# Optimization experiments

Hardware: AMD Instinct MI355X
Metric: run time of the kernel (lower is better)

## Reference

```python
import jax, jax.numpy as jnp
import numpy as np

B, T, C, H = 4, 2048, 2048, 16
HD = C // H


def apply_rope(x, cos, sin):
    d = x.shape[-1]
    neg_half = jnp.concatenate([-x[..., d // 2:], x[..., :d // 2]], axis=-1)
    return x * cos + neg_half * sin


def setup_inputs() -> dict:
    key = jax.random.key(0)
    ks = jax.random.split(key, 12)
    s = 1.0 / np.sqrt(C)
    return {
        "x": jax.random.normal(ks[0], (B, T, C), jnp.float32),
        "cos": jax.random.uniform(ks[1], (T, C), jnp.float32),
        "sin": jax.random.uniform(ks[2], (T, C), jnp.float32),
        "Wq": jax.random.normal(ks[3], (C, C), jnp.float32) * s,
        "bq": jnp.zeros((C,), jnp.float32),
        "Wk": jax.random.normal(ks[4], (C, C), jnp.float32) * s,
        "bk": jnp.zeros((C,), jnp.float32),
        "Wv": jax.random.normal(ks[5], (C, C), jnp.float32) * s,
        "bv": jnp.zeros((C,), jnp.float32),
        "Wo": jax.random.normal(ks[6], (C, C), jnp.float32) * s,
        "bo": jnp.zeros((C,), jnp.float32),
    }


def reference(x, cos, sin, Wq, bq, Wk, bk, Wv, bv, Wo, bo):
    # projections (torch Linear: x @ W.T + b)
    q = x @ Wq.T + bq
    k = x @ Wk.T + bk
    v = x @ Wv.T + bv
    # kv cache stores PRE-RoPE k and v (as in the original)
    k_new, v_new = k, v
    # RoPE on the full embedding dim, before head split
    q = apply_rope(q, cos[:T], sin[:T])
    k = apply_rope(k, cos[:T], sin[:T])
    # split heads -> [B, H, T, HD]
    qh = q.reshape(B, T, H, HD).transpose(0, 2, 1, 3)
    kh = k.reshape(B, T, H, HD).transpose(0, 2, 1, 3)
    vh = v.reshape(B, T, H, HD).transpose(0, 2, 1, 3)
    scores = jnp.einsum("bhqd,bhkd->bhqk", qh, kh) / jnp.sqrt(jnp.float32(HD))
    causal = jnp.tril(jnp.ones((T, T), bool))
    scores = jnp.where(causal, scores, jnp.float32(-jnp.inf))
    attn = jax.nn.softmax(scores, axis=-1)
    out = jnp.einsum("bhqk,bhkd->bhqd", attn, vh)
    out = out.transpose(0, 2, 1, 3).reshape(B, T, C)
    out = out @ Wo.T + bo
    return (out, k_new, v_new)
```

## Files before the change

kernel.cpp:

```cpp
#include <hip/hip_runtime.h>

typedef unsigned short u16;
typedef unsigned int u32;

typedef __attribute__((ext_vector_type(8))) short bf16x8;
typedef __attribute__((ext_vector_type(4))) float f32x4;
typedef __attribute__((ext_vector_type(16))) float f32x16;
typedef __attribute__((ext_vector_type(4))) u32 u32x4;

__device__ __forceinline__ u16 f2bf(float f) {
  u32 u = __builtin_bit_cast(u32, f);
  u32 r = (u + 0x7fffu + ((u >> 16) & 1u)) >> 16;
  return (u16)r;
}
__device__ __forceinline__ float bf2f(u16 h) {
  return __builtin_bit_cast(float, (u32)h << 16);
}
__device__ __forceinline__ u32 cvtpk(float lo, float hi) {
  u32 d;
  asm("v_cvt_pk_bf16_f32 %0, %1, %2" : "=v"(d) : "v"(lo), "v"(hi));
  return d;
}
__device__ __forceinline__ void plswap(u32& a, u32& b) {
  asm("v_permlane32_swap_b32 %0, %1" : "+v"(a), "+v"(b));
}

#define GLD16(g, l)                                       \
  __builtin_amdgcn_global_load_lds(                       \
      (__attribute__((address_space(1))) void*)(g),       \
      (__attribute__((address_space(3))) void*)(l), 16, 0, 0)

#define WAITV8() asm volatile("s_waitcnt vmcnt(8)" ::: "memory")
#define WAITV0() asm volatile("s_waitcnt vmcnt(0)" ::: "memory")
#define BARF()                               \
  {                                          \
    asm volatile("" ::: "memory");           \
    __builtin_amdgcn_s_barrier();            \
    asm volatile("" ::: "memory");           \
  }

__global__ __launch_bounds__(256) void cvt_bf16(const float* __restrict__ src,
                                                u16* __restrict__ dst, int n4) {
  int i = blockIdx.x * 256 + threadIdx.x;
  if (i >= n4) return;
  float4 v = ((const float4*)src)[i];
  ushort4 o;
  o.x = f2bf(v.x); o.y = f2bf(v.y); o.z = f2bf(v.z); o.w = f2bf(v.w);
  ((ushort4*)dst)[i] = o;
}

__global__ __launch_bounds__(256) void cvt_w4(const float* __restrict__ s0,
                                              const float* __restrict__ s1,
                                              const float* __restrict__ s2,
                                              const float* __restrict__ s3,
                                              u16* __restrict__ d0,
                                              u16* __restrict__ d1,
                                              u16* __restrict__ d2,
                                              u16* __restrict__ d3) {
  int j = blockIdx.x >> 12;
  int i = (blockIdx.x & 4095) * 256 + threadIdx.x;
  const float* src = (j == 0) ? s0 : (j == 1) ? s1 : (j == 2) ? s2 : s3;
  u16* dst = (j == 0) ? d0 : (j == 1) ? d1 : (j == 2) ? d2 : d3;
  float4 v = ((const float4*)src)[i];
  ushort4 o;
  o.x = f2bf(v.x); o.y = f2bf(v.y); o.z = f2bf(v.z); o.w = f2bf(v.w);
  ((ushort4*)dst)[i] = o;
}

__global__ __launch_bounds__(256) void rope2(u16* __restrict__ qb,
                                             u16* __restrict__ kb,
                                             const float* __restrict__ cosT,
                                             const float* __restrict__ sinT,
                                             float scaleQ) {
  int i = blockIdx.x * 256 + threadIdx.x;
  int c4 = (i & 255) << 2;
  size_t bt = (size_t)(i >> 8);
  int t = (int)(bt & 2047);
  float4 c1 = *(const float4*)&cosT[(size_t)t * 2048 + c4];
  float4 s1 = *(const float4*)&sinT[(size_t)t * 2048 + c4];
  float4 c2 = *(const float4*)&cosT[(size_t)t * 2048 + c4 + 1024];
  float4 s2 = *(const float4*)&sinT[(size_t)t * 2048 + c4 + 1024];
#pragma unroll
  for (int which = 0; which < 2; which++) {
    u16* buf = which ? kb : qb;
    float scale = which ? 1.0f : scaleQ;
    u16* p1 = buf + bt * 2048 + c4;
    u16* p2 = p1 + 1024;
    ushort4 x1 = *(const ushort4*)p1;
    ushort4 x2 = *(const ushort4*)p2;
    float a0 = bf2f(x1.x), a1 = bf2f(x1.y), a2 = bf2f(x1.z), a3 = bf2f(x1.w);
    float b0 = bf2f(x2.x), b1 = bf2f(x2.y), b2 = bf2f(x2.z), b3 = bf2f(x2.w);
    ushort4 o1, o2;
    o1.x = f2bf((a0 * c1.x - b0 * s1.x) * scale);
    o1.y = f2bf((a1 * c1.y - b1 * s1.y) * scale);
    o1.z = f2bf((a2 * c1.z - b2 * s1.z) * scale);
    o1.w = f2bf((a3 * c1.w - b3 * s1.w) * scale);
    o2.x = f2bf((b0 * c2.x + a0 * s2.x) * scale);
    o2.y = f2bf((b1 * c2.y + a1 * s2.y) * scale);
    o2.z = f2bf((b2 * c2.z + a2 * s2.z) * scale);
    o2.w = f2bf((b3 * c2.w + a3 * s2.w) * scale);
    *(ushort4*)p1 = o1;
    *(ushort4*)p2 = o2;
  }
}

__global__ __launch_bounds__(512, 2) void gemm_bt(const u16* __restrict__ A,
                                                  const u16* __restrict__ Wm,
                                                  const float* __restrict__ bias,
                                                  float* __restrict__ outF,
                                                  u16* __restrict__ outB,
                                                  u16* __restrict__ outT) {
  __shared__ __attribute__((aligned(16))) char L[131072];
  const int tid = threadIdx.x;
  const int lane = tid & 63;
  const int w = tid >> 6;
  const int wr = w >> 2;
  const int wcn = w & 3;
  const int lin = blockIdx.y * 8 + blockIdx.x;
  const int swz = ((lin & 7) << 5) | (lin >> 3);
  const int m0 = (swz >> 3) * 256, n0 = (swz & 7) * 256;
  const int r15 = lane & 15, rg = lane >> 4;
  const int sw = (r15 & 7) << 4;

  const int trow = tid >> 3;
  const int tlog = ((tid & 7) << 4) ^ ((trow & 7) << 4);
  const u16* pA = A + (size_t)(m0 + trow) * 2048 + (tlog >> 1);
  const u16* pB = Wm + (size_t)(n0 + trow) * 2048 + (tlog >> 1);
  char* dA = L + tid * 16;
  char* dB = L + 65536 + tid * 16;

#define STAGE(dst, src, koff)                                   \
  {                                                             \
    _Pragma("unroll")                                           \
    for (int c = 0; c < 4; c++)                                 \
      GLD16((src) + (size_t)c * 131072 + (koff), (dst) + c * 8192); \
  }

  const char* aBase = L + wr * 16384;
  const char* bBase = L + 65536 + (wcn >> 1) * 16384 + (wcn & 1) * 8192;

  f32x4 acc[8][4] = {};
  bf16x8 ar[4][2], br[2][2][2];

  auto LD_A = [&](int mq, int soff) {
#pragma unroll
    for (int mf = 0; mf < 4; mf++)
#pragma unroll
      for (int ks = 0; ks < 2; ks++) {
        int row = mq * 64 + mf * 16 + r15;
        ar[mf][ks] = *(const bf16x8*)(aBase + soff + row * 128 +
                                      ((ks * 64 + rg * 16) ^ sw));
      }
  };
  auto LD_B = [&](int nq, int soff) {
#pragma unroll
    for (int nf = 0; nf < 2; nf++)
#pragma unroll
      for (int ks = 0; ks < 2; ks++) {
        int row = nq * 32 + nf * 16 + r15;
        br[nq][nf][ks] = *(const bf16x8*)(bBase + soff + row * 128 +
                                          ((ks * 64 + rg * 16) ^ sw));
      }
  };
  auto QUAD = [&](int mq, int nq) {
#pragma unroll
    for (int mf = 0; mf < 4; mf++)
#pragma unroll
      for (int nf = 0; nf < 2; nf++)
#pragma unroll
        for (int ks = 0; ks < 2; ks++)
          acc[mq * 4 + mf][nq * 2 + nf] = __builtin_amdgcn_mfma_f32_16x16x32_bf16(
              ar[mf][ks], br[nq][nf][ks], acc[mq * 4 + mf][nq * 2 + nf], 0, 0, 0);
  };
  auto COMPUTE = [&](int soff) {
    LD_A(0, soff);
    LD_B(0, soff);
    LD_B(1, soff);
    __builtin_amdgcn_s_setprio(1);
    QUAD(0, 0);
    QUAD(0, 1);
    __builtin_amdgcn_s_setprio(0);
    LD_A(1, soff);
    __builtin_amdgcn_s_setprio(1);
    QUAD(1, 1);
    QUAD(1, 0);
    __builtin_amdgcn_s_setprio(0);
  };

  STAGE(dA, pA, 0);
  STAGE(dB, pB, 0);
  asm volatile("" ::: "memory");
  STAGE(dA + 32768, pA, 64);
  STAGE(dB + 32768, pB, 64);
  WAITV8();
  BARF();

  for (int it = 0; it < 16; it++) {
    COMPUTE(0);
    BARF();
    if (it < 15) {
      STAGE(dA, pA, (2 * it + 2) * 64);
      STAGE(dB, pB, (2 * it + 2) * 64);
      WAITV8();
    } else {
      WAITV0();
    }
    BARF();
    COMPUTE(32768);
    if (it < 15) {
      BARF();
      STAGE(dA + 32768, pA, (2 * it + 3) * 64);
      STAGE(dB + 32768, pB, (2 * it + 3) * 64);
      WAITV8();
      BARF();
    }
  }

#pragma unroll
  for (int am = 0; am < 8; am++)
#pragma unroll
    for (int bn = 0; bn < 4; bn++) {
      int n = n0 + wcn * 64 + bn * 16 + r15;
      float bs = bias[n];
#pragma unroll
      for (int i = 0; i < 4; i++) {
        int m = m0 + wr * 128 + am * 16 + rg * 4 + i;
        float v = acc[am][bn][i] + bs;
        if (outF) outF[(size_t)m * 2048 + n] = v;
        if (outB) outB[(size_t)m * 2048 + n] = f2bf(v);
        if (outT) {
          int b_ = m >> 11, t_ = m & 2047, h_ = n >> 7, d_ = n & 127;
          outT[(((size_t)(b_ * 16 + h_) * 128 + d_) << 11) + t_] = f2bf(v);
        }
      }
    }
#undef STAGE
}

__global__ __launch_bounds__(256, 2) void attn_fwd(const u16* __restrict__ Qb,
                                                   const u16* __restrict__ Kb,
                                                   const u16* __restrict__ Vt,
                                                   u16* __restrict__ AO) {
  __shared__ __attribute__((aligned(16))) u16 Ks[2][64 * 128];
  __shared__ __attribute__((aligned(16))) u16 Vs[2][64 * 128];
  const int tid = threadIdx.x;
  const int lane = tid & 63;
  const int w = tid >> 6;
  const int c31 = lane & 31, hi = lane >> 5;
  const int bh = blockIdx.y;
  const int b = bh >> 4, h = bh & 15;
  const int p = blockIdx.x;

  const u16* ksrc[4];
  const u16* vsrc[4];
  int xoff[4];
#pragma unroll
  for (int c = 0; c < 4; c++) {
    int X = c * 4096 + tid * 16;
    int row = X >> 8, phys = X & 255;
    int lg = phys ^ ((row & 15) << 4);
    xoff[c] = X;
    ksrc[c] = Kb + (size_t)(b * 2048 + row) * 2048 + h * 128 + (lg >> 1);
    int vd = row + ((lg >> 7) << 6);
    int kvb = lg & 127;
    vsrc[c] = Vt + ((size_t)(b * 16 + h) * 128 + vd) * 2048 + (kvb >> 1);
  }

  for (int phase = 0; phase < 2; phase++) {
    const int q0 = (phase == 0 ? (15 - p) : p) * 128;
    const int qw0 = q0 + w * 32;
    const int q = qw0 + c31;

    bf16x8 qreg[8];
    {
      const u16* qp = Qb + ((size_t)(b * 2048 + q)) * 2048 + h * 128 + hi * 8;
#pragma unroll
      for (int ks = 0; ks < 8; ks++) qreg[ks] = *(const bf16x8*)(qp + ks * 16);
    }

    f32x16 accO[4] = {};
    float m_run = -__builtin_inff(), l_run = 0.f;
    const int ntiles = (q0 >> 6) + 2;

    __syncthreads();
#pragma unroll
    for (int c = 0; c < 4; c++) {
      GLD16(ksrc[c], (char*)Ks + xoff[c]);
      GLD16(vsrc[c], (char*)Vs + xoff[c]);
    }

    for (int it = 0; it < ntiles; it++) {
      const int kv0 = it << 6;
      const int buf = it & 1;
      __syncthreads();
      if (it + 1 < ntiles) {
        const int nb = buf ^ 1;
        const int kvn = (it + 1) << 6;
#pragma unroll
        for (int c = 0; c < 4; c++) {
          GLD16(ksrc[c] + (size_t)kvn * 2048, (char*)Ks + nb * 16384 + xoff[c]);
          GLD16(vsrc[c] + kvn, (char*)Vs + nb * 16384 + xoff[c]);
        }
      }
      if (kv0 > qw0 + 31) continue;

      f32x16 sT[2] = {};
      {
        const char* kb = (const char*)Ks + buf * 16384;
#pragma unroll
        for (int kvt = 0; kvt < 2; kvt++) {
          int krow = kvt * 32 + c31;
          const char* kr = kb + krow * 256;
          int swz = (krow & 15) << 4;
#pragma unroll
          for (int ks = 0; ks < 8; ks++) {
            bf16x8 kf = *(const bf16x8*)(kr + ((ks * 32 + hi * 16) ^ swz));
            sT[kvt] = __builtin_amdgcn_mfma_f32_32x32x16_bf16(kf, qreg[ks], sT[kvt], 0, 0, 0);
          }
        }
      }

      if (kv0 + 63 > qw0) {
#pragma unroll
        for (int kvt = 0; kvt < 2; kvt++)
#pragma unroll
          for (int r = 0; r < 16; r++) {
            int kv = kv0 + kvt * 32 + (r & 3) + 8 * (r >> 2) + 4 * hi;
            if (kv > q) sT[kvt][r] = -__builtin_inff();
          }
      }

      float tm[16];
#pragma unroll
      for (int r = 0; r < 16; r++) tm[r] = fmaxf(sT[0][r], sT[1][r]);
#pragma unroll
      for (int st = 8; st > 0; st >>= 1)
#pragma unroll
        for (int r = 0; r < st; r++) tm[r] = fmaxf(tm[r], tm[r + st]);
      float pmax = tm[0];
      pmax = fmaxf(pmax, __shfl_xor(pmax, 32));

      if (!__all(pmax - m_run <= 8.0f)) {
        float mnew = fmaxf(m_run, pmax);
        float alpha = exp2f(m_run - mnew);
        m_run = mnew;
        l_run *= alpha;
#pragma unroll
        for (int r = 0; r < 16; r++) {
          float ar = __shfl(alpha, (r & 3) + 8 * (r >> 2) + 4 * hi);
#pragma unroll
          for (int dt = 0; dt < 4; dt++) accO[dt][r] *= ar;
        }
      }

      float a0 = 0.f, a1 = 0.f, a2 = 0.f, a3 = 0.f;
#pragma unroll
      for (int kvt = 0; kvt < 2; kvt++)
#pragma unroll
        for (int r = 0; r < 16; r++) {
          float pv = exp2f(sT[kvt][r] - m_run);
          sT[kvt][r] = pv;
          if ((r & 3) == 0) a0 += pv; else if ((r & 3) == 1) a1 += pv;
          else if ((r & 3) == 2) a2 += pv; else a3 += pv;
        }
      float rs = (a0 + a1) + (a2 + a3);
      rs += __shfl_xor(rs, 32);
      l_run += rs;

      u32x4 pa[4];
#pragma unroll
      for (int kvt = 0; kvt < 2; kvt++)
#pragma unroll
        for (int hf = 0; hf < 2; hf++) {
          u32 wA0 = cvtpk(sT[kvt][hf * 8 + 0], sT[kvt][hf * 8 + 1]);
          u32 wA1 = cvtpk(sT[kvt][hf * 8 + 4], sT[kvt][hf * 8 + 5]);
          u32 wB0 = cvtpk(sT[kvt][hf * 8 + 2], sT[kvt][hf * 8 + 3]);
          u32 wB1 = cvtpk(sT[kvt][hf * 8 + 6], sT[kvt][hf * 8 + 7]);
          plswap(wA0, wA1);
          plswap(wB0, wB1);
          pa[kvt * 2 + hf] = (u32x4){wA0, wB0, wA1, wB1};
        }

      {
        const char* vb = (const char*)Vs + buf * 16384;
#pragma unroll
        for (int dt = 0; dt < 4; dt++) {
          int vrow = (dt & 1) * 32 + c31;
          const char* vr = vb + vrow * 256;
          int swz = (vrow & 15) << 4;
          int hsel = (dt >> 1) * 128;
#pragma unroll
          for (int ks = 0; ks < 4; ks++) {
            bf16x8 vf = *(const bf16x8*)(vr + ((hsel + ks * 32 + hi * 16) ^ swz));
            bf16x8 paf = __builtin_bit_cast(bf16x8, pa[ks]);
            accO[dt] = __builtin_amdgcn_mfma_f32_32x32x16_bf16(paf, vf, accO[dt], 0, 0, 0);
          }
        }
      }
    }

    float linv = 1.0f / l_run;
#pragma unroll
    for (int r = 0; r < 16; r++) {
      int crow = (r & 3) + 8 * (r >> 2) + 4 * hi;
      float lr = __shfl(linv, crow);
      int qq = qw0 + crow;
      u16* op = AO + (size_t)(b * 2048 + qq) * 2048 + h * 128 + c31;
#pragma unroll
      for (int dt = 0; dt < 4; dt++) op[dt * 32] = f2bf(accO[dt][r] * lr);
    }
  }
}

extern "C" void kernel_launch(void* const* d_in, const int* in_sizes, int n_in,
                              void* d_out, int out_size, void* d_ws, size_t ws_size,
                              hipStream_t stream) {
  const float* x    = (const float*)d_in[0];
  const float* cosT = (const float*)d_in[1];
  const float* sinT = (const float*)d_in[2];
  const float* Wq   = (const float*)d_in[3];
  const float* bq   = (const float*)d_in[4];
  const float* Wk   = (const float*)d_in[5];
  const float* bk   = (const float*)d_in[6];
  const float* Wv   = (const float*)d_in[7];
  const float* bv   = (const float*)d_in[8];
  const float* Wo   = (const float*)d_in[9];
  const float* bo   = (const float*)d_in[10];

  float* out   = (float*)d_out;
  float* k_new = out + (size_t)16777216;
  float* v_new = out + (size_t)33554432;

  char* ws = (char*)d_ws;
  u16* xb  = (u16*)(ws);
  u16* Wqb = (u16*)(ws + 33554432);
  u16* Wkb = (u16*)(ws + 41943040);
  u16* Wvb = (u16*)(ws + 50331648);
  u16* Wob = (u16*)(ws + 58720256);
  u16* Qb  = (u16*)(ws + 67108864);
  u16* Kb  = (u16*)(ws + 100663296);
  u16* Vt  = (u16*)(ws + 134217728);
  u16* AO  = xb;

  cvt_bf16<<<16384, 256, 0, stream>>>(x, xb, 4194304);
  cvt_w4<<<16384, 256, 0, stream>>>(Wq, Wk, Wv, Wo, Wqb, Wkb, Wvb, Wob);

  dim3 gg(8, 32);
  gemm_bt<<<gg, 512, 0, stream>>>(xb, Wqb, bq, nullptr, Qb, nullptr);
  gemm_bt<<<gg, 512, 0, stream>>>(xb, Wkb, bk, k_new, Kb, nullptr);
  gemm_bt<<<gg, 512, 0, stream>>>(xb, Wvb, bv, v_new, nullptr, Vt);

  const float sc2 = 1.44269504088896f * 0.08838834764831845f;
  rope2<<<8192, 256, 0, stream>>>(Qb, Kb, cosT, sinT, sc2);

  attn_fwd<<<dim3(8, 64), 256, 0, stream>>>(Qb, Kb, Vt, AO);

  gemm_bt<<<gg, 512, 0, stream>>>(AO, Wob, bo, out, nullptr, nullptr);
}
```

Before: 475.4 us.

## Fuse Q/K/V projections into one GEMM launch and enlarge attention blocks

The three separate Q, K and V projection GEMMs become one launch over a 24x32 tile grid. Each tile selects its bias and output format (bf16 Q, fp32+bf16 K, fp32+transposed bf16 V) by which weight segment it covers, which relies on Wq/Wk/Wv being contiguous in the workspace. The attention kernel moves to 512 threads with 256-query blocks sharing K/V tiles, halving per-thread loads and the block count. This removes launch gaps and tail effects and increases K/V reuse, but the larger attention blocks carry more idle causal work and lower occupancy.

```diff
diff --git a/kernel.cpp b/kernel.cpp
--- a/kernel.cpp
+++ b/kernel.cpp
@@ -104,30 +104,91 @@
   }
 }
 
-__global__ __launch_bounds__(512, 2) void gemm_bt(const u16* __restrict__ A,
-                                                  const u16* __restrict__ Wm,
-                                                  const float* __restrict__ bias,
-                                                  float* __restrict__ outF,
-                                                  u16* __restrict__ outB,
-                                                  u16* __restrict__ outT) {
-  __shared__ __attribute__((aligned(16))) char L[131072];
-  const int tid = threadIdx.x;
-  const int lane = tid & 63;
-  const int w = tid >> 6;
-  const int wr = w >> 2;
-  const int wcn = w & 3;
-  const int lin = blockIdx.y * 8 + blockIdx.x;
-  const int swz = ((lin & 7) << 5) | (lin >> 3);
-  const int m0 = (swz >> 3) * 256, n0 = (swz & 7) * 256;
-  const int r15 = lane & 15, rg = lane >> 4;
-  const int sw = (r15 & 7) << 4;
-
-  const int trow = tid >> 3;
-  const int tlog = ((tid & 7) << 4) ^ ((trow & 7) << 4);
-  const u16* pA = A + (size_t)(m0 + trow) * 2048 + (tlog >> 1);
-  const u16* pB = Wm + (size_t)(n0 + trow) * 2048 + (tlog >> 1);
-  char* dA = L + tid * 16;
-  char* dB = L + 65536 + tid * 16;
+#define GEMM_CORE(Aptr, Wptr)                                                  \
+  __shared__ __attribute__((aligned(16))) char L[131072];                      \
+  const int tid = threadIdx.x;                                                 \
+  const int lane = tid & 63;                                                   \
+  const int w = tid >> 6;                                                      \
+  const int wr = w >> 2;                                                       \
+  const int wcn = w & 3;                                                       \
+  const int r15 = lane & 15, rg = lane >> 4;                                   \
+  const int sw = (r15 & 7) << 4;                                               \
+  const int trow = tid >> 3;                                                   \
+  const int tlog = ((tid & 7) << 4) ^ ((trow & 7) << 4);                       \
+  const u16* pA = (Aptr) + (size_t)(m0 + trow) * 2048 + (tlog >> 1);           \
+  const u16* pB = (Wptr) + (size_t)(n0 + trow) * 2048 + (tlog >> 1);           \
+  char* dA = L + tid * 16;                                                     \
+  char* dB = L + 65536 + tid * 16;                                             \
+  const char* aBase = L + wr * 16384;                                          \
+  const char* bBase = L + 65536 + (wcn >> 1) * 16384 + (wcn & 1) * 8192;       \
+  f32x4 acc[8][4] = {};                                                        \
+  bf16x8 ar[4][2], br[2][2][2];                                                \
+  auto LD_A = [&](int mq, int soff) {                                          \
+    _Pragma("unroll") for (int mf = 0; mf < 4; mf++)                           \
+        _Pragma("unroll") for (int ks = 0; ks < 2; ks++) {                     \
+      int row = mq * 64 + mf * 16 + r15;                                       \
+      ar[mf][ks] = *(const bf16x8*)(aBase + soff + row * 128 +                 \
+                                    ((ks * 64 + rg * 16) ^ sw));               \
+    }                                                                          \
+  };                                                                           \
+  auto LD_B = [&](int nq, int soff) {                                          \
+    _Pragma("unroll") for (int nf = 0; nf < 2; nf++)                           \
+        _Pragma("unroll") for (int ks = 0; ks < 2; ks++) {                     \
+      int row = nq * 32 + nf * 16 + r15;                                       \
+      br[nq][nf][ks] = *(const bf16x8*)(bBase + soff + row * 128 +             \
+                                        ((ks * 64 + rg * 16) ^ sw));           \
+    }                                                                          \
+  };                                                                           \
+  auto QUAD = [&](int mq, int nq) {                                            \
+    _Pragma("unroll") for (int mf = 0; mf < 4; mf++)                           \
+        _Pragma("unroll") for (int nf = 0; nf < 2; nf++)                       \
+            _Pragma("unroll") for (int ks = 0; ks < 2; ks++)                   \
+        acc[mq * 4 + mf][nq * 2 + nf] =                                        \
+            __builtin_amdgcn_mfma_f32_16x16x32_bf16(                           \
+                ar[mf][ks], br[nq][nf][ks], acc[mq * 4 + mf][nq * 2 + nf],     \
+                0, 0, 0);                                                      \
+  };                                                                           \
+  auto COMPUTE = [&](int soff) {                                               \
+    LD_A(0, soff);                                                             \
+    LD_B(0, soff);                                                             \
+    LD_B(1, soff);                                                             \
+    __builtin_amdgcn_s_setprio(1);                                             \
+    QUAD(0, 0);                                                                \
+    QUAD(0, 1);                                                                \
+    __builtin_amdgcn_s_setprio(0);                                             \
+    LD_A(1, soff);                                                             \
+    __builtin_amdgcn_s_setprio(1);                                             \
+    QUAD(1, 1);                                                                \
+    QUAD(1, 0);                                                                \
+    __builtin_amdgcn_s_setprio(0);                                             \
+  };                                                                           \
+  STAGE(dA, pA, 0);                                                            \
+  STAGE(dB, pB, 0);                                                            \
+  asm volatile("" ::: "memory");                                               \
+  STAGE(dA + 32768, pA, 64);                                                   \
+  STAGE(dB + 32768, pB, 64);                                                   \
+  WAITV8();                                                                    \
+  BARF();                                                                      \
+  for (int it = 0; it < 16; it++) {                                            \
+    COMPUTE(0);                                                                \
+    BARF();                                                                    \
+    if (it < 15) {                                                             \
+      STAGE(dA, pA, (2 * it + 2) * 64);                                        \
+      STAGE(dB, pB, (2 * it + 2) * 64);                                        \
+      WAITV8();                                                                \
+    } else {                                                                   \
+      WAITV0();                                                                \
+    }                                                                          \
+    BARF();                                                                    \
+    COMPUTE(32768);                                                            \
+    if (it < 15) {                                                             \
+      BARF();                                                                  \
+      STAGE(dA + 32768, pA, (2 * it + 3) * 64);                                \
+      STAGE(dB + 32768, pB, (2 * it + 3) * 64);                                \
+      WAITV8();                                                                \
+      BARF();                                                                  \
+    }                                                                          \
+  }
 
 #define STAGE(dst, src, koff)                                   \
   {                                                             \
@@ -136,86 +197,55 @@
       GLD16((src) + (size_t)c * 131072 + (koff), (dst) + c * 8192); \
   }
 
-  const char* aBase = L + wr * 16384;
-  const char* bBase = L + 65536 + (wcn >> 1) * 16384 + (wcn & 1) * 8192;
-
-  f32x4 acc[8][4] = {};
-  bf16x8 ar[4][2], br[2][2][2];
-
-  auto LD_A = [&](int mq, int soff) {
-#pragma unroll
-    for (int mf = 0; mf < 4; mf++)
-#pragma unroll
-      for (int ks = 0; ks < 2; ks++) {
-        int row = mq * 64 + mf * 16 + r15;
-        ar[mf][ks] = *(const bf16x8*)(aBase + soff + row * 128 +
-                                      ((ks * 64 + rg * 16) ^ sw));
-      }
-  };
-  auto LD_B = [&](int nq, int soff) {
-#pragma unroll
-    for (int nf = 0; nf < 2; nf++)
-#pragma unroll
-      for (int ks = 0; ks < 2; ks++) {
-        int row = nq * 32 + nf * 16 + r15;
-        br[nq][nf][ks] = *(const bf16x8*)(bBase + soff + row * 128 +
-                                          ((ks * 64 + rg * 16) ^ sw));
-      }
-  };
-  auto QUAD = [&](int mq, int nq) {
-#pragma unroll
-    for (int mf = 0; mf < 4; mf++)
-#pragma unroll
-      for (int nf = 0; nf < 2; nf++)
-#pragma unroll
-        for (int ks = 0; ks < 2; ks++)
-          acc[mq * 4 + mf][nq * 2 + nf] = __builtin_amdgcn_mfma_f32_16x16x32_bf16(
-              ar[mf][ks], br[nq][nf][ks], acc[mq * 4 + mf][nq * 2 + nf], 0, 0, 0);
-  };
-  auto COMPUTE = [&](int soff) {
-    LD_A(0, soff);
-    LD_B(0, soff);
-    LD_B(1, soff);
-    __builtin_amdgcn_s_setprio(1);
-    QUAD(0, 0);
-    QUAD(0, 1);
-    __builtin_amdgcn_s_setprio(0);
-    LD_A(1, soff);
-    __builtin_amdgcn_s_setprio(1);
-    QUAD(1, 1);
-    QUAD(1, 0);
-    __builtin_amdgcn_s_setprio(0);
-  };
-
-  STAGE(dA, pA, 0);
-  STAGE(dB, pB, 0);
-  asm volatile("" ::: "memory");
-  STAGE(dA + 32768, pA, 64);
-  STAGE(dB + 32768, pB, 64);
-  WAITV8();
-  BARF();
-
-  for (int it = 0; it < 16; it++) {
-    COMPUTE(0);
-    BARF();
-    if (it < 15) {
-      STAGE(dA, pA, (2 * it + 2) * 64);
-      STAGE(dB, pB, (2 * it + 2) * 64);
-      WAITV8();
-    } else {
-      WAITV0();
-    }
-    BARF();
-    COMPUTE(32768);
-    if (it < 15) {
-      BARF();
-      STAGE(dA + 32768, pA, (2 * it + 3) * 64);
-      STAGE(dB + 32768, pB, (2 * it + 3) * 64);
-      WAITV8();
-      BARF();
-    }
-  }
-
+__global__ __launch_bounds__(512, 2) void gemm_qkv(const u16* __restrict__ A,
+                                                   const u16* __restrict__ Wqkv,
+                                                   const float* __restrict__ bq,
+                                                   const float* __restrict__ bk,
+                                                   const float* __restrict__ bv,
+                                                   u16* __restrict__ Qb,
+                                                   float* __restrict__ k_new,
+                                                   u16* __restrict__ Kb,
+                                                   float* __restrict__ v_new,
+                                                   u16* __restrict__ Vt) {
+  const int lin = blockIdx.y * 24 + blockIdx.x;
+  const int swz = (lin & 7) * 96 + (lin >> 3);
+  const int m0 = (swz / 24) * 256, n0 = (swz % 24) * 256;
+  GEMM_CORE(A, Wqkv)
+  const int seg = n0 >> 11;
+  const float* bias = (seg == 0) ? bq : (seg == 1) ? bk : bv;
+#pragma unroll
+  for (int am = 0; am < 8; am++)
+#pragma unroll
+    for (int bn = 0; bn < 4; bn++) {
+      int n = n0 + wcn * 64 + bn * 16 + r15;
+      int nl = n & 2047;
+      float bs = bias[nl];
+#pragma unroll
+      for (int i = 0; i < 4; i++) {
+        int m = m0 + wr * 128 + am * 16 + rg * 4 + i;
+        float v = acc[am][bn][i] + bs;
+        if (seg == 0) {
+          Qb[(size_t)m * 2048 + nl] = f2bf(v);
+        } else if (seg == 1) {
+          k_new[(size_t)m * 2048 + nl] = v;
+          Kb[(size_t)m * 2048 + nl] = f2bf(v);
+        } else {
+          v_new[(size_t)m * 2048 + nl] = v;
+          int b_ = m >> 11, t_ = m & 2047, h_ = nl >> 7, d_ = nl & 127;
+          Vt[(((size_t)(b_ * 16 + h_) * 128 + d_) << 11) + t_] = f2bf(v);
+        }
+      }
+    }
+}
+
+__global__ __launch_bounds__(512, 2) void gemm_bt(const u16* __restrict__ A,
+                                                  const u16* __restrict__ Wm,
+                                                  const float* __restrict__ bias,
+                                                  float* __restrict__ outF) {
+  const int lin = blockIdx.y * 8 + blockIdx.x;
+  const int swzb = ((lin & 7) << 5) | (lin >> 3);
+  const int m0 = (swzb >> 3) * 256, n0 = (swzb & 7) * 256;
+  GEMM_CORE(A, Wm)
 #pragma unroll
   for (int am = 0; am < 8; am++)
 #pragma unroll
@@ -225,19 +255,14 @@
 #pragma unroll
       for (int i = 0; i < 4; i++) {
         int m = m0 + wr * 128 + am * 16 + rg * 4 + i;
-        float v = acc[am][bn][i] + bs;
-        if (outF) outF[(size_t)m * 2048 + n] = v;
-        if (outB) outB[(size_t)m * 2048 + n] = f2bf(v);
-        if (outT) {
-          int b_ = m >> 11, t_ = m & 2047, h_ = n >> 7, d_ = n & 127;
-          outT[(((size_t)(b_ * 16 + h_) * 128 + d_) << 11) + t_] = f2bf(v);
-        }
-      }
-    }
+        outF[(size_t)m * 2048 + n] = acc[am][bn][i] + bs;
+      }
+    }
+}
 #undef STAGE
-}
-
-__global__ __launch_bounds__(256, 2) void attn_fwd(const u16* __restrict__ Qb,
+#undef GEMM_CORE
+
+__global__ __launch_bounds__(512, 2) void attn_fwd(const u16* __restrict__ Qb,
                                                    const u16* __restrict__ Kb,
                                                    const u16* __restrict__ Vt,
                                                    u16* __restrict__ AO) {
@@ -251,12 +276,12 @@
   const int b = bh >> 4, h = bh & 15;
   const int p = blockIdx.x;
 
-  const u16* ksrc[4];
-  const u16* vsrc[4];
-  int xoff[4];
-#pragma unroll
-  for (int c = 0; c < 4; c++) {
-    int X = c * 4096 + tid * 16;
+  const u16* ksrc[2];
+  const u16* vsrc[2];
+  int xoff[2];
+#pragma unroll
+  for (int c = 0; c < 2; c++) {
+    int X = c * 8192 + tid * 16;
     int row = X >> 8, phys = X & 255;
     int lg = phys ^ ((row & 15) << 4);
     xoff[c] = X;
@@ -267,7 +292,7 @@
   }
 
   for (int phase = 0; phase < 2; phase++) {
-    const int q0 = (phase == 0 ? (15 - p) : p) * 128;
+    const int q0 = (phase == 0 ? (7 - p) : p) * 256;
     const int qw0 = q0 + w * 32;
     const int q = qw0 + c31;
 
@@ -280,11 +305,11 @@
 
     f32x16 accO[4] = {};
     float m_run = -__builtin_inff(), l_run = 0.f;
-    const int ntiles = (q0 >> 6) + 2;
+    const int ntiles = (q0 >> 6) + 4;
 
     __syncthreads();
 #pragma unroll
-    for (int c = 0; c < 4; c++) {
+    for (int c = 0; c < 2; c++) {
       GLD16(ksrc[c], (char*)Ks + xoff[c]);
       GLD16(vsrc[c], (char*)Vs + xoff[c]);
     }
@@ -297,7 +322,7 @@
         const int nb = buf ^ 1;
         const int kvn = (it + 1) << 6;
 #pragma unroll
-        for (int c = 0; c < 4; c++) {
+        for (int c = 0; c < 2; c++) {
           GLD16(ksrc[c] + (size_t)kvn * 2048, (char*)Ks + nb * 16384 + xoff[c]);
           GLD16(vsrc[c] + kvn, (char*)Vs + nb * 16384 + xoff[c]);
         }
@@ -445,15 +470,13 @@
   cvt_bf16<<<16384, 256, 0, stream>>>(x, xb, 4194304);
   cvt_w4<<<16384, 256, 0, stream>>>(Wq, Wk, Wv, Wo, Wqb, Wkb, Wvb, Wob);
 
-  dim3 gg(8, 32);
-  gemm_bt<<<gg, 512, 0, stream>>>(xb, Wqb, bq, nullptr, Qb, nullptr);
-  gemm_bt<<<gg, 512, 0, stream>>>(xb, Wkb, bk, k_new, Kb, nullptr);
-  gemm_bt<<<gg, 512, 0, stream>>>(xb, Wvb, bv, v_new, nullptr, Vt);
+  gemm_qkv<<<dim3(24, 32), 512, 0, stream>>>(xb, Wqb, bq, bk, bv,
+                                             Qb, k_new, Kb, v_new, Vt);
 
   const float sc2 = 1.44269504088896f * 0.08838834764831845f;
   rope2<<<8192, 256, 0, stream>>>(Qb, Kb, cosT, sinT, sc2);
 
-  attn_fwd<<<dim3(8, 64), 256, 0, stream>>>(Qb, Kb, Vt, AO);
-
-  gemm_bt<<<gg, 512, 0, stream>>>(AO, Wob, bo, out, nullptr, nullptr);
-}
+  attn_fwd<<<dim3(4, 64), 512, 0, stream>>>(Qb, Kb, Vt, AO);
+
+  gemm_bt<<<dim3(8, 32), 512, 0, stream>>>(AO, Wob, bo, out);
+}
```

New measurement: 477.9 us. About the same (+0.5%).
